# Performance work log

Hardware: AMD Instinct MI355X
Metric: run time of the kernel (lower is better)

Reference implementation:

```python
import jax, jax.numpy as jnp
import numpy as np

B, S, D, H = 4, 2048, 1024, 16
HD = D // H
ROPE_THETA = 10000.0


def setup_inputs() -> dict:
    key = jax.random.key(0)
    ks = jax.random.split(key, 5)
    scale = 1.0 / np.sqrt(D)
    inp = {
        "x": jax.random.normal(ks[0], (B, S, D), dtype=jnp.float32),
        "Wq": jax.random.normal(ks[1], (D, D), dtype=jnp.float32) * scale,
        "bq": jnp.zeros((D,), jnp.float32),
        "Wk": jax.random.normal(ks[2], (D, D), dtype=jnp.float32) * scale,
        "bk": jnp.zeros((D,), jnp.float32),
        "Wv": jax.random.normal(ks[3], (D, D), dtype=jnp.float32) * scale,
        "bv": jnp.zeros((D,), jnp.float32),
        "Wo": jax.random.normal(ks[4], (D, D), dtype=jnp.float32) * scale,
        "bo": jnp.zeros((D,), jnp.float32),
        # causal mask: True means masked (j > i), matching masked_fill semantics
        "attn_mask": jnp.triu(jnp.ones((S, S), dtype=bool), k=1),
    }
    return inp


def _rope(x):
    # x: [B, H, S, HD]; half-split rotary embedding
    half = HD // 2
    inv_freq = 1.0 / (ROPE_THETA ** (jnp.arange(0, half, dtype=jnp.float32) / half))
    pos = jnp.arange(x.shape[2], dtype=jnp.float32)
    freqs = pos[:, None] * inv_freq[None, :]            # [S, half]
    cos = jnp.cos(freqs)[None, None]                    # [1,1,S,half]
    sin = jnp.sin(freqs)[None, None]
    x1, x2 = x[..., :half], x[..., half:]
    return jnp.concatenate([x1 * cos - x2 * sin, x2 * cos + x1 * sin], axis=-1)


def reference(x, Wq, bq, Wk, bk, Wv, bv, Wo, bo, attn_mask):
    def shape(t):  # [B,S,D] -> [B,H,S,HD]
        return t.reshape(B, S, H, HD).transpose(0, 2, 1, 3)

    q = shape(x @ Wq.T + bq)
    k = shape(x @ Wk.T + bk)
    v = shape(x @ Wv.T + bv)
    q = _rope(q)
    k = _rope(k)
    scores = jnp.einsum("bhqd,bhkd->bhqk", q, k) * (HD ** -0.5)
    scores = jnp.where(attn_mask[None, None], -jnp.inf, scores)
    w = jax.nn.softmax(scores, axis=-1)
    attn = jnp.einsum("bhqk,bhkd->bhqd", w, v)
    merged = attn.transpose(0, 2, 1, 3).reshape(B, S, D)
    return merged @ Wo.T + bo
```

## Files before the change

kernel.cpp:

```cpp
#include <hip/hip_runtime.h>
#include <math.h>

#define BATCH 4
#define SEQ   2048
#define DMODEL 1024
#define NHEAD 16
#define HDIM  64
#define MROWS (BATCH*SEQ)

typedef unsigned short u16;
typedef unsigned int   u32;

using bf16x8 = __attribute__((ext_vector_type(8))) short;
using f32x4  = __attribute__((ext_vector_type(4))) float;
using f32x16 = __attribute__((ext_vector_type(16))) float;

__device__ __forceinline__ u16 f2bf(float f) {
    u32 u = __float_as_uint(f);
    u += 0x7fffu + ((u >> 16) & 1u);
    return (u16)(u >> 16);
}
__device__ __forceinline__ u32 pack2bf(float a, float b) {
    u32 ua = __float_as_uint(a); ua += 0x7fffu + ((ua >> 16) & 1u);
    u32 ub = __float_as_uint(b); ub += 0x7fffu + ((ub >> 16) & 1u);
    return (ua >> 16) | (ub & 0xffff0000u);
}

#define GLOBAL_LOAD_LDS16(gp, lp)                                              \
    __builtin_amdgcn_global_load_lds(                                          \
        (const __attribute__((address_space(1))) void*)(gp),                   \
        (__attribute__((address_space(3))) void*)(lp), 16, 0, 0)

__global__ __launch_bounds__(256) void convert_inputs(
    const float* __restrict__ x,  const float* __restrict__ wq,
    const float* __restrict__ wk, const float* __restrict__ wv,
    const float* __restrict__ wo, u16* __restrict__ dst)
{
    long long i4 = ((long long)blockIdx.x * 256 + threadIdx.x) * 4;
    const float* src; long long off;
    if (i4 < 8388608LL) { src = x; off = i4; }
    else {
        long long j = i4 - 8388608LL;
        int seg = (int)(j >> 20);
        off = j & 1048575LL;
        src = (seg == 0) ? wq : (seg == 1) ? wk : (seg == 2) ? wv : wo;
    }
    float4 v = *(const float4*)(src + off);
    u32 lo = (u32)f2bf(v.x) | ((u32)f2bf(v.y) << 16);
    u32 hi = (u32)f2bf(v.z) | ((u32)f2bf(v.w) << 16);
    *(uint2*)(dst + i4) = make_uint2(lo, hi);
}

template<int QKV>
__global__ __launch_bounds__(512) void gemm_mfma(
    const u16* __restrict__ A,
    const u16* __restrict__ Wq_, const u16* __restrict__ Wk_, const u16* __restrict__ Wv_,
    const float* __restrict__ bq_, const float* __restrict__ bk_, const float* __restrict__ bv_,
    u16* __restrict__ Cq_, u16* __restrict__ Ck_, u16* __restrict__ Cv_,
    float* __restrict__ Cf)
{
    __shared__ u16 As[3 * 256 * 64];
    __shared__ u16 Ws[3 * 128 * 64];

    const int t    = threadIdx.x;
    const int lane = t & 63;
    const int w    = t >> 6;
    const int quad = lane >> 4;
    const int l15  = lane & 15;
    const int wm   = w >> 1;
    const int wn   = w & 1;

    const int bx  = blockIdx.x;
    const int xcd = bx & 7;
    const int i_  = bx >> 3;
    const int bml = i_ & 3;
    const int n_  = i_ >> 2;
    const int seg = (QKV ? (n_ >> 3) : 0);
    const int nn  = (QKV ? (n_ & 7) : n_);

    const u16*   W    = (seg == 0) ? Wq_ : (seg == 1) ? Wk_ : Wv_;
    const float* bias = (seg == 0) ? bq_ : (seg == 1) ? bk_ : bv_;
    u16*         Cb   = (seg == 0) ? Cq_ : (seg == 1) ? Ck_ : Cv_;

    const int bm   = (xcd * 4 + bml) * 256;
    const int bn   = nn * 128;
    const int wrow = wm * 64;
    const int wcol = wn * 64;

    const int sr8 = lane >> 3;
    const int scl = (lane & 7) ^ sr8;
    const u16* gA = A + (size_t)(bm + 8 * w + sr8) * DMODEL + scl * 8;
    const u16* gB = W + (size_t)(bn + 8 * w + sr8) * DMODEL + scl * 8;

#define STAGE_A(li, kt, bs)                                                    \
    GLOBAL_LOAD_LDS16(gA + (size_t)(li) * 64 * DMODEL + (kt) * 64,             \
                      &As[(bs) * 16384 + ((li) * 64 + 8 * w) * 64])
#define STAGE_B(li, kt, bs)                                                    \
    GLOBAL_LOAD_LDS16(gB + (size_t)(li) * 64 * DMODEL + (kt) * 64,             \
                      &Ws[(bs) * 8192 + ((li) * 64 + 8 * w) * 64])

    STAGE_A(0, 0, 0); STAGE_A(1, 0, 0); STAGE_A(2, 0, 0); STAGE_A(3, 0, 0);
    STAGE_B(0, 0, 0); STAGE_B(1, 0, 0);
    STAGE_A(0, 1, 1); STAGE_A(1, 1, 1); STAGE_A(2, 1, 1); STAGE_A(3, 1, 1);
    STAGE_B(0, 1, 1); STAGE_B(1, 1, 1);
    asm volatile("s_waitcnt vmcnt(6)" ::: "memory");
    __builtin_amdgcn_s_barrier();

    const int c0 = (quad ^ (l15 & 7)) * 8;
    const int c1 = c0 ^ 32;

    f32x4 acc[4][4] = {};

    int bsel = 0;
    for (int kt = 0; kt < DMODEL / 64; ++kt) {
        const u16* Ab = &As[bsel * 16384];
        const u16* Bb = &Ws[bsel * 8192];
        const int  ks = kt + 2;
        const int  sb = (bsel >= 1) ? bsel - 1 : 2;
        const bool st = (ks < DMODEL / 64);

        bf16x8 af[4], bf[4];

        #pragma unroll
        for (int i = 0; i < 4; ++i)
            af[i] = *(const bf16x8*)&Ab[(wrow + 16 * i + l15) * 64 + c0];
        #pragma unroll
        for (int j = 0; j < 4; ++j)
            bf[j] = *(const bf16x8*)&Bb[(wcol + 16 * j + l15) * 64 + c0];
        if (st) { STAGE_A(0, ks, sb); STAGE_A(1, ks, sb); STAGE_A(2, ks, sb); }
        __builtin_amdgcn_s_barrier();
        __builtin_amdgcn_s_setprio(1);
        #pragma unroll
        for (int i = 0; i < 4; ++i)
            #pragma unroll
            for (int j = 0; j < 4; ++j)
                acc[i][j] = __builtin_amdgcn_mfma_f32_16x16x32_bf16(af[i], bf[j], acc[i][j], 0, 0, 0);
        __builtin_amdgcn_s_setprio(0);
        __builtin_amdgcn_s_barrier();

        #pragma unroll
        for (int i = 0; i < 4; ++i)
            af[i] = *(const bf16x8*)&Ab[(wrow + 16 * i + l15) * 64 + c1];
        #pragma unroll
        for (int j = 0; j < 4; ++j)
            bf[j] = *(const bf16x8*)&Bb[(wcol + 16 * j + l15) * 64 + c1];
        if (st) { STAGE_A(3, ks, sb); STAGE_B(0, ks, sb); STAGE_B(1, ks, sb); }
        __builtin_amdgcn_s_barrier();
        __builtin_amdgcn_s_setprio(1);
        #pragma unroll
        for (int i = 0; i < 4; ++i)
            #pragma unroll
            for (int j = 0; j < 4; ++j)
                acc[i][j] = __builtin_amdgcn_mfma_f32_16x16x32_bf16(af[i], bf[j], acc[i][j], 0, 0, 0);
        __builtin_amdgcn_s_setprio(0);
        if (st) asm volatile("s_waitcnt vmcnt(6)" ::: "memory");
        else    asm volatile("s_waitcnt vmcnt(0)" ::: "memory");
        __builtin_amdgcn_s_barrier();

        bsel = (bsel == 2) ? 0 : bsel + 1;
    }
#undef STAGE_A
#undef STAGE_B

    float bv[4];
    #pragma unroll
    for (int j = 0; j < 4; j++) bv[j] = bias[bn + wcol + 16 * j + l15];

    if constexpr (QKV == 0) {
        #pragma unroll
        for (int i = 0; i < 4; i++)
            #pragma unroll
            for (int r = 0; r < 4; r++) {
                int mg = bm + wrow + 16 * i + quad * 4 + r;
                #pragma unroll
                for (int j = 0; j < 4; j++)
                    Cf[(size_t)mg * DMODEL + bn + wcol + 16 * j + l15] = acc[i][j][r] + bv[j];
            }
    } else {
        if (seg == 2) {
            #pragma unroll
            for (int i = 0; i < 4; i++)
                #pragma unroll
                for (int r = 0; r < 4; r++) {
                    int mg = bm + wrow + 16 * i + quad * 4 + r;
                    #pragma unroll
                    for (int j = 0; j < 4; j++)
                        Cb[(size_t)mg * DMODEL + bn + wcol + 16 * j + l15] = f2bf(acc[i][j][r] + bv[j]);
                }
        } else {
            const float qscale = (seg == 0) ? 0.125f : 1.0f;
            float inv[2];
            #pragma unroll
            for (int j = 0; j < 2; j++) {
                int d = 16 * j + l15;
                inv[j] = exp2f(-(float)d * 0.4152410118609203f);
            }
            #pragma unroll
            for (int i = 0; i < 4; i++)
                #pragma unroll
                for (int r = 0; r < 4; r++) {
                    int mg = bm + wrow + 16 * i + quad * 4 + r;
                    int s  = mg & (SEQ - 1);
                    #pragma unroll
                    for (int j = 0; j < 2; j++) {
                        float f = (float)s * inv[j];
                        float sn, cs;
                        __sincosf(f, &sn, &cs);
                        float a1 = acc[i][j][r]     + bv[j];
                        float a2 = acc[i][j + 2][r] + bv[j + 2];
                        float o1 = (a1 * cs - a2 * sn) * qscale;
                        float o2 = (a2 * cs + a1 * sn) * qscale;
                        Cb[(size_t)mg * DMODEL + bn + wcol + 16 * j       + l15] = f2bf(o1);
                        Cb[(size_t)mg * DMODEL + bn + wcol + 16 * (j + 2) + l15] = f2bf(o2);
                    }
                }
        }
    }
}

__global__ __launch_bounds__(256) void attn_mfma(
    const u16* __restrict__ Q, const u16* __restrict__ K,
    const u16* __restrict__ V, u16* __restrict__ O)
{
    __shared__ u16 Qs[128 * 64];
    __shared__ u16 Ks[64 * 64];
    __shared__ u16 Vt[64 * 64];
    __shared__ u16 Ps[128 * 64];
    __shared__ float lS[128];

    const int t    = threadIdx.x;
    const int lane = t & 63;
    const int w    = t >> 6;
    const int l31  = lane & 31;
    const int hl   = lane >> 5;
    const int bid  = blockIdx.x;
    const int bh   = bid & 63;
    const int qt   = 15 - (bid >> 6);
    const int h    = bh & (NHEAD - 1);
    const int b    = bh >> 4;
    const int q0   = qt * 128;

    const size_t gbase = ((size_t)b * SEQ) * DMODEL + h * HDIM;

    {
        int rl = lane >> 3, cp = lane & 7;
        int c  = cp ^ rl;
        #pragma unroll
        for (int i = 0; i < 4; i++) {
            int row = 32 * w + 8 * i + rl;
            GLOBAL_LOAD_LDS16(Q + gbase + (size_t)(q0 + row) * DMODEL + c * 8,
                              &Qs[(32 * w + 8 * i) * 64]);
        }
    }
    __syncthreads();

    bf16x8 qf[4];
    {
        int row = 32 * w + l31;
        #pragma unroll
        for (int s = 0; s < 4; s++) {
            int c = (hl + 2 * s) ^ (row & 7);
            qf[s] = *(const bf16x8*)&Qs[row * 64 + c * 8];
        }
    }

    float lsum = 0.0f;
    f32x16 oacc[2] = {};

    const int ktn = 2 * qt + 2;
    for (int kt = 0; kt < ktn; kt++) {
        const int k0 = kt * 64;
        __syncthreads();

        {
            int rl = lane >> 3, cp = lane & 7;
            int c  = cp ^ rl;
            #pragma unroll
            for (int i = 0; i < 2; i++) {
                int row = 16 * w + 8 * i + rl;
                GLOBAL_LOAD_LDS16(K + gbase + (size_t)(k0 + row) * DMODEL + c * 8,
                                  &Ks[(16 * w + 8 * i) * 64]);
            }
        }
        {
            int j0 = (t & 31) * 2, d0 = (t >> 5) * 8;
            uint4 va = *(const uint4*)(V + gbase + (size_t)(k0 + j0)     * DMODEL + d0);
            uint4 vb = *(const uint4*)(V + gbase + (size_t)(k0 + j0 + 1) * DMODEL + d0);
            const u16* pa = (const u16*)&va;
            const u16* pb = (const u16*)&vb;
            int jd = t & 31, pos = jd & 3, ch = jd >> 2;
            #pragma unroll
            for (int e = 0; e < 8; e++) {
                int row = d0 + e;
                int pcch = ch ^ (row & 7);
                *(u32*)&Vt[row * 64 + pcch * 8 + pos * 2] = (u32)pa[e] | ((u32)pb[e] << 16);
            }
        }
        __syncthreads();

        const bool act = (k0 <= q0 + 32 * w + 31);
        if (act) {
            const int qrow = 32 * w + l31;
            const int qg   = q0 + qrow;
            #pragma unroll
            for (int krh = 0; krh < 2; krh++) {
                const bool qact = (k0 + 32 * krh <= q0 + 32 * w + 31);
                if (!qact) {
                    #pragma unroll
                    for (int g = 0; g < 4; g++)
                        #pragma unroll
                        for (int pp = 0; pp < 2; pp++) {
                            int kr = 32 * krh + 8 * g + 4 * hl + 2 * pp;
                            int jd = kr >> 1;
                            int pcc = (jd >> 2) ^ (qrow & 7);
                            *(u32*)&Ps[qrow * 64 + pcc * 8 + (jd & 3) * 2] = 0u;
                        }
                    continue;
                }
                f32x16 s = {};
                #pragma unroll
                for (int stp = 0; stp < 4; stp++) {
                    int row = 32 * krh + l31;
                    int c   = (hl + 2 * stp) ^ (l31 & 7);
                    bf16x8 ka = *(const bf16x8*)&Ks[row * 64 + c * 8];
                    s = __builtin_amdgcn_mfma_f32_32x32x16_bf16(ka, qf[stp], s, 0, 0, 0);
                }
                if (k0 + 32 * krh + 31 > q0 + 32 * w) {
                    #pragma unroll
                    for (int r = 0; r < 16; r++) {
                        int krg = k0 + 32 * krh + (r & 3) + 8 * (r >> 2) + 4 * hl;
                        if (krg > qg) s[r] = -1e30f;
                    }
                }
                float pv[16];
                #pragma unroll
                for (int r = 0; r < 16; r++) { pv[r] = __expf(s[r]); lsum += pv[r]; }
                #pragma unroll
                for (int g = 0; g < 4; g++)
                    #pragma unroll
                    for (int pp = 0; pp < 2; pp++) {
                        int kr = 32 * krh + 8 * g + 4 * hl + 2 * pp;
                        int jd = kr >> 1;
                        int pcc = (jd >> 2) ^ (qrow & 7);
                        *(u32*)&Ps[qrow * 64 + pcc * 8 + (jd & 3) * 2] =
                            pack2bf(pv[4 * g + 2 * pp], pv[4 * g + 2 * pp + 1]);
                    }
            }

            #pragma unroll
            for (int stp = 0; stp < 4; stp++) {
                int c = (hl + 2 * stp) ^ (l31 & 7);
                bf16x8 pf = *(const bf16x8*)&Ps[qrow * 64 + c * 8];
                #pragma unroll
                for (int dh = 0; dh < 2; dh++) {
                    bf16x8 vf = *(const bf16x8*)&Vt[(32 * dh + l31) * 64 + c * 8];
                    oacc[dh] = __builtin_amdgcn_mfma_f32_32x32x16_bf16(pf, vf, oacc[dh], 0, 0, 0);
                }
            }
        }
    }

    lsum += __shfl_xor(lsum, 32, 64);
    if (lane < 32) lS[32 * w + lane] = lsum;
    __syncthreads();

    #pragma unroll
    for (int g = 0; g < 4; g++) {
        f32x4 lv = *(const f32x4*)&lS[32 * w + 8 * g + 4 * hl];
        #pragma unroll
        for (int rr = 0; rr < 4; rr++) {
            int qg = q0 + 32 * w + rr + 8 * g + 4 * hl;
            float inv = 1.0f / lv[rr];
            #pragma unroll
            for (int dh = 0; dh < 2; dh++) {
                float o = oacc[dh][4 * g + rr] * inv;
                O[gbase + (size_t)qg * DMODEL + 32 * dh + l31] = f2bf(o);
            }
        }
    }
}

extern "C" void kernel_launch(void* const* d_in, const int* in_sizes, int n_in,
                              void* d_out, int out_size, void* d_ws, size_t ws_size,
                              hipStream_t stream)
{
    const float* x  = (const float*)d_in[0];
    const float* Wq = (const float*)d_in[1];
    const float* bq = (const float*)d_in[2];
    const float* Wk = (const float*)d_in[3];
    const float* bk = (const float*)d_in[4];
    const float* Wv = (const float*)d_in[5];
    const float* bv = (const float*)d_in[6];
    const float* Wo = (const float*)d_in[7];
    const float* bo = (const float*)d_in[8];

    u16* wsp = (u16*)d_ws;
    u16* xb  = wsp;
    u16* Wqb = wsp + 8388608;
    u16* Wkb = Wqb + 1048576;
    u16* Wvb = Wkb + 1048576;
    u16* Wob = Wvb + 1048576;
    u16* Qb  = Wob + 1048576;
    u16* Kb  = Qb + 8388608;
    u16* Vb  = Kb + 8388608;
    u16* Ab  = Vb + 8388608;

    convert_inputs<<<12288, 256, 0, stream>>>(x, Wq, Wk, Wv, Wo, xb);

    gemm_mfma<1><<<768, 512, 0, stream>>>(xb, Wqb, Wkb, Wvb, bq, bk, bv,
                                          Qb, Kb, Vb, nullptr);

    attn_mfma<<<1024, 256, 0, stream>>>(Qb, Kb, Vb, Ab);

    gemm_mfma<0><<<256, 512, 0, stream>>>(Ab, Wob, nullptr, nullptr, bo, nullptr, nullptr,
                                          nullptr, nullptr, nullptr, (float*)d_out);
}
```

Measured before the change: 263.4 us.

## Double-buffer K/V in attention, pre-transpose V in projection, keep P in registers

The V projection epilogue now stages results through LDS and writes V transposed as [B,H,HD,S], so the attention kernel can load V tiles directly into LDS with async global_load_lds. K and V tiles are double-buffered, with the next tile prefetched while the current one is computed, and there is a single barrier per iteration. The P matrix is packed with v_cvt_pk_bf16 and rearranged with permlane32_swap in registers instead of going through LDS. Also in the change: exp is replaced by exp2 with log2e folded into the Q scale, priority hints are set around the MFMAs, and the block order is reshuffled for better load balance. The new code relies on the aliasing of Qs with the second buffer being safe after the added sync, and on the ISA-specific asm instructions.

New measurement: 254.6 us. -3.3%, faster.

```diff
diff --git a/kernel.cpp b/kernel.cpp
--- a/kernel.cpp
+++ b/kernel.cpp
@@ -14,6 +14,7 @@
 using bf16x8 = __attribute__((ext_vector_type(8))) short;
 using f32x4  = __attribute__((ext_vector_type(4))) float;
 using f32x16 = __attribute__((ext_vector_type(16))) float;
+using u32x4  = __attribute__((ext_vector_type(4))) unsigned int;
 
 __device__ __forceinline__ u16 f2bf(float f) {
     u32 u = __float_as_uint(f);
@@ -25,6 +26,12 @@
     u32 ub = __float_as_uint(b); ub += 0x7fffu + ((ub >> 16) & 1u);
     return (ua >> 16) | (ub & 0xffff0000u);
 }
+__device__ __forceinline__ u32 cvtpk(float a, float b) {
+    u32 r;
+    asm("v_cvt_pk_bf16_f32 %0, %1, %2" : "=v"(r) : "v"(a), "v"(b));
+    return r;
+}
+#define PLSWAP(a, b) asm("v_permlane32_swap_b32 %0, %1" : "+v"(a), "+v"(b))
 
 #define GLOBAL_LOAD_LDS16(gp, lp)                                              \
     __builtin_amdgcn_global_load_lds(                                          \
@@ -178,17 +185,36 @@
             }
     } else {
         if (seg == 2) {
-            #pragma unroll
-            for (int i = 0; i < 4; i++)
+            u16* T = As;
+            #pragma unroll
+            for (int i = 0; i < 4; i++) {
                 #pragma unroll
-                for (int r = 0; r < 4; r++) {
-                    int mg = bm + wrow + 16 * i + quad * 4 + r;
-                    #pragma unroll
-                    for (int j = 0; j < 4; j++)
-                        Cb[(size_t)mg * DMODEL + bn + wcol + 16 * j + l15] = f2bf(acc[i][j][r] + bv[j]);
+                for (int j = 0; j < 4; j++) {
+                    int col = wrow + 16 * i + quad * 4;
+                    int row = wcol + 16 * j + l15;
+                    u32 lo = pack2bf(acc[i][j][0] + bv[j], acc[i][j][1] + bv[j]);
+                    u32 hi = pack2bf(acc[i][j][2] + bv[j], acc[i][j][3] + bv[j]);
+                    *(uint2*)((char*)T + row * 512 + ((col * 2) ^ ((row & 3) << 4)))
+                        = make_uint2(lo, hi);
                 }
+            }
+            __syncthreads();
+            {
+                int row  = t >> 2, colc = t & 3;
+                int hgl  = (bn + row) >> 6;
+                int dl   = (bn + row) & 63;
+                int bb   = bm >> 11;
+                size_t obase = (((size_t)(bb * NHEAD + hgl)) * HDIM + dl) * SEQ
+                             + (bm & (SEQ - 1)) + colc * 64;
+                #pragma unroll
+                for (int k = 0; k < 8; k++) {
+                    uint4 vv = *(const uint4*)((const char*)T + row * 512
+                                 + ((colc * 128 + k * 16) ^ ((row & 3) << 4)));
+                    *(uint4*)(Cb + obase + k * 8) = vv;
+                }
+            }
         } else {
-            const float qscale = (seg == 0) ? 0.125f : 1.0f;
+            const float qscale = (seg == 0) ? 0.18033688011112042f : 1.0f;
             float inv[2];
             #pragma unroll
             for (int j = 0; j < 2; j++) {
@@ -220,13 +246,15 @@
 
 __global__ __launch_bounds__(256) void attn_mfma(
     const u16* __restrict__ Q, const u16* __restrict__ K,
-    const u16* __restrict__ V, u16* __restrict__ O)
+    const u16* __restrict__ VT, u16* __restrict__ O)
 {
-    __shared__ u16 Qs[128 * 64];
-    __shared__ u16 Ks[64 * 64];
-    __shared__ u16 Vt[64 * 64];
-    __shared__ u16 Ps[128 * 64];
-    __shared__ float lS[128];
+    __shared__ __align__(16) u16 smem[16640];
+    u16* const Qs  = smem;
+    u16* const Ks0 = smem + 8192;
+    u16* const Ks1 = smem;
+    u16* const Vt0 = smem + 12288;
+    u16* const Vt1 = smem + 4096;
+    float* const lS = (float*)(smem + 16384);
 
     const int t    = threadIdx.x;
     const int lane = t & 63;
@@ -235,22 +263,32 @@
     const int hl   = lane >> 5;
     const int bid  = blockIdx.x;
     const int bh   = bid & 63;
-    const int qt   = 15 - (bid >> 6);
+    const int x_   = bid >> 6, g_ = x_ >> 2, r_ = x_ & 3;
+    const int qt   = (g_ == 0) ? 15 - r_ : (g_ == 1) ? 8 + r_
+                   : (g_ == 2) ? 4 + r_ : 3 - r_;
     const int h    = bh & (NHEAD - 1);
     const int b    = bh >> 4;
     const int q0   = qt * 128;
 
     const size_t gbase = ((size_t)b * SEQ) * DMODEL + h * HDIM;
-
-    {
-        int rl = lane >> 3, cp = lane & 7;
-        int c  = cp ^ rl;
-        #pragma unroll
-        for (int i = 0; i < 4; i++) {
-            int row = 32 * w + 8 * i + rl;
-            GLOBAL_LOAD_LDS16(Q + gbase + (size_t)(q0 + row) * DMODEL + c * 8,
-                              &Qs[(32 * w + 8 * i) * 64]);
-        }
+    const size_t vbase = ((size_t)(b * NHEAD + h)) * HDIM * SEQ;
+
+    const int rl  = lane >> 3;
+    const int csw = (lane & 7) ^ rl;
+
+    #pragma unroll
+    for (int i = 0; i < 4; i++) {
+        int row = 32 * w + 8 * i + rl;
+        GLOBAL_LOAD_LDS16(Q + gbase + (size_t)(q0 + row) * DMODEL + csw * 8,
+                          &Qs[(32 * w + 8 * i) * 64]);
+    }
+    #pragma unroll
+    for (int i = 0; i < 2; i++) {
+        int row = 16 * w + 8 * i + rl;
+        GLOBAL_LOAD_LDS16(K + gbase + (size_t)row * DMODEL + csw * 8,
+                          &Ks0[(16 * w + 8 * i) * 64]);
+        GLOBAL_LOAD_LDS16(VT + vbase + (size_t)row * SEQ + csw * 8,
+                          &Vt0[(16 * w + 8 * i) * 64]);
     }
     __syncthreads();
 
@@ -263,102 +301,94 @@
             qf[s] = *(const bf16x8*)&Qs[row * 64 + c * 8];
         }
     }
+    __syncthreads();
 
     float lsum = 0.0f;
     f32x16 oacc[2] = {};
+    const int qg   = q0 + 32 * w + l31;
+    const int qmax = q0 + 32 * w + 31;
+
+#define QUADRANT(KRH, F0, F1) do {                                             \
+    f32x16 s_ = {};                                                            \
+    __builtin_amdgcn_s_setprio(1);                                             \
+    _Pragma("unroll")                                                          \
+    for (int stp_ = 0; stp_ < 4; ++stp_) {                                     \
+        int c_ = ((hl + 2 * stp_) ^ (l31 & 7)) * 8;                            \
+        bf16x8 ka_ = *(const bf16x8*)&Ksb[(32 * (KRH) + l31) * 64 + c_];       \
+        s_ = __builtin_amdgcn_mfma_f32_32x32x16_bf16(ka_, qf[stp_], s_, 0, 0, 0);\
+    }                                                                          \
+    __builtin_amdgcn_s_setprio(0);                                             \
+    if (k0 + 32 * (KRH) + 31 > q0 + 32 * w) {                                  \
+        _Pragma("unroll")                                                      \
+        for (int rr_ = 0; rr_ < 16; ++rr_) {                                   \
+            int krg_ = k0 + 32 * (KRH) + (rr_ & 3) + 8 * (rr_ >> 2) + 4 * hl;  \
+            if (krg_ > qg) s_[rr_] = -1e30f;                                   \
+        }                                                                      \
+    }                                                                          \
+    float pv_[16];                                                             \
+    _Pragma("unroll")                                                          \
+    for (int rr_ = 0; rr_ < 16; ++rr_) pv_[rr_] = __builtin_amdgcn_exp2f(s_[rr_]);\
+    lsum += ((pv_[0]+pv_[1])+(pv_[2]+pv_[3])) + ((pv_[4]+pv_[5])+(pv_[6]+pv_[7]))\
+          + ((pv_[8]+pv_[9])+(pv_[10]+pv_[11])) + ((pv_[12]+pv_[13])+(pv_[14]+pv_[15]));\
+    u32 k01_ = cvtpk(pv_[0], pv_[1]),   k23_ = cvtpk(pv_[2], pv_[3]);          \
+    u32 k45_ = cvtpk(pv_[4], pv_[5]),   k67_ = cvtpk(pv_[6], pv_[7]);          \
+    u32 k89_ = cvtpk(pv_[8], pv_[9]),   kab_ = cvtpk(pv_[10], pv_[11]);        \
+    u32 kcd_ = cvtpk(pv_[12], pv_[13]), kef_ = cvtpk(pv_[14], pv_[15]);        \
+    PLSWAP(k01_, k45_); PLSWAP(k23_, k67_);                                    \
+    PLSWAP(k89_, kcd_); PLSWAP(kab_, kef_);                                    \
+    { union { u32x4 u; bf16x8 v; } c0_; c0_.u = (u32x4){k01_, k23_, k45_, k67_};\
+      F0 = c0_.v; }                                                            \
+    { union { u32x4 u; bf16x8 v; } c1_; c1_.u = (u32x4){k89_, kab_, kcd_, kef_};\
+      F1 = c1_.v; }                                                            \
+} while (0)
+
+#define PVSTEP(STP, PF) do {                                                   \
+    int c_ = ((hl + 2 * (STP)) ^ (l31 & 7)) * 8;                               \
+    bf16x8 v0_ = *(const bf16x8*)&Vtb[l31 * 64 + c_];                          \
+    bf16x8 v1_ = *(const bf16x8*)&Vtb[(32 + l31) * 64 + c_];                   \
+    oacc[0] = __builtin_amdgcn_mfma_f32_32x32x16_bf16(PF, v0_, oacc[0], 0, 0, 0);\
+    oacc[1] = __builtin_amdgcn_mfma_f32_32x32x16_bf16(PF, v1_, oacc[1], 0, 0, 0);\
+} while (0)
 
     const int ktn = 2 * qt + 2;
     for (int kt = 0; kt < ktn; kt++) {
         const int k0 = kt * 64;
-        __syncthreads();
-
-        {
-            int rl = lane >> 3, cp = lane & 7;
-            int c  = cp ^ rl;
+        u16* const Ksb = (kt & 1) ? Ks1 : Ks0;
+        u16* const Vtb = (kt & 1) ? Vt1 : Vt0;
+
+        if (kt + 1 < ktn) {
+            u16* const Ksn = (kt & 1) ? Ks0 : Ks1;
+            u16* const Vtn = (kt & 1) ? Vt0 : Vt1;
+            const size_t kk0 = (size_t)(kt + 1) * 64;
             #pragma unroll
             for (int i = 0; i < 2; i++) {
                 int row = 16 * w + 8 * i + rl;
-                GLOBAL_LOAD_LDS16(K + gbase + (size_t)(k0 + row) * DMODEL + c * 8,
-                                  &Ks[(16 * w + 8 * i) * 64]);
+                GLOBAL_LOAD_LDS16(K + gbase + (kk0 + row) * DMODEL + csw * 8,
+                                  &Ksn[(16 * w + 8 * i) * 64]);
+                GLOBAL_LOAD_LDS16(VT + vbase + (size_t)row * SEQ + kk0 + csw * 8,
+                                  &Vtn[(16 * w + 8 * i) * 64]);
             }
         }
-        {
-            int j0 = (t & 31) * 2, d0 = (t >> 5) * 8;
-            uint4 va = *(const uint4*)(V + gbase + (size_t)(k0 + j0)     * DMODEL + d0);
-            uint4 vb = *(const uint4*)(V + gbase + (size_t)(k0 + j0 + 1) * DMODEL + d0);
-            const u16* pa = (const u16*)&va;
-            const u16* pb = (const u16*)&vb;
-            int jd = t & 31, pos = jd & 3, ch = jd >> 2;
-            #pragma unroll
-            for (int e = 0; e < 8; e++) {
-                int row = d0 + e;
-                int pcch = ch ^ (row & 7);
-                *(u32*)&Vt[row * 64 + pcch * 8 + pos * 2] = (u32)pa[e] | ((u32)pb[e] << 16);
+
+        if (k0 <= qmax) {
+            const bool q2 = (k0 + 32 <= qmax);
+            bf16x8 pa0, pa1, pa2, pa3;
+            QUADRANT(0, pa0, pa1);
+            __builtin_amdgcn_s_setprio(1);
+            PVSTEP(0, pa0); PVSTEP(1, pa1);
+            __builtin_amdgcn_s_setprio(0);
+            if (q2) {
+                QUADRANT(1, pa2, pa3);
+                __builtin_amdgcn_s_setprio(1);
+                PVSTEP(2, pa2); PVSTEP(3, pa3);
+                __builtin_amdgcn_s_setprio(0);
             }
         }
-        __syncthreads();
-
-        const bool act = (k0 <= q0 + 32 * w + 31);
-        if (act) {
-            const int qrow = 32 * w + l31;
-            const int qg   = q0 + qrow;
-            #pragma unroll
-            for (int krh = 0; krh < 2; krh++) {
-                const bool qact = (k0 + 32 * krh <= q0 + 32 * w + 31);
-                if (!qact) {
-                    #pragma unroll
-                    for (int g = 0; g < 4; g++)
-                        #pragma unroll
-                        for (int pp = 0; pp < 2; pp++) {
-                            int kr = 32 * krh + 8 * g + 4 * hl + 2 * pp;
-                            int jd = kr >> 1;
-                            int pcc = (jd >> 2) ^ (qrow & 7);
-                            *(u32*)&Ps[qrow * 64 + pcc * 8 + (jd & 3) * 2] = 0u;
-                        }
-                    continue;
-                }
-                f32x16 s = {};
-                #pragma unroll
-                for (int stp = 0; stp < 4; stp++) {
-                    int row = 32 * krh + l31;
-                    int c   = (hl + 2 * stp) ^ (l31 & 7);
-                    bf16x8 ka = *(const bf16x8*)&Ks[row * 64 + c * 8];
-                    s = __builtin_amdgcn_mfma_f32_32x32x16_bf16(ka, qf[stp], s, 0, 0, 0);
-                }
-                if (k0 + 32 * krh + 31 > q0 + 32 * w) {
-                    #pragma unroll
-                    for (int r = 0; r < 16; r++) {
-                        int krg = k0 + 32 * krh + (r & 3) + 8 * (r >> 2) + 4 * hl;
-                        if (krg > qg) s[r] = -1e30f;
-                    }
-                }
-                float pv[16];
-                #pragma unroll
-                for (int r = 0; r < 16; r++) { pv[r] = __expf(s[r]); lsum += pv[r]; }
-                #pragma unroll
-                for (int g = 0; g < 4; g++)
-                    #pragma unroll
-                    for (int pp = 0; pp < 2; pp++) {
-                        int kr = 32 * krh + 8 * g + 4 * hl + 2 * pp;
-                        int jd = kr >> 1;
-                        int pcc = (jd >> 2) ^ (qrow & 7);
-                        *(u32*)&Ps[qrow * 64 + pcc * 8 + (jd & 3) * 2] =
-                            pack2bf(pv[4 * g + 2 * pp], pv[4 * g + 2 * pp + 1]);
-                    }
-            }
-
-            #pragma unroll
-            for (int stp = 0; stp < 4; stp++) {
-                int c = (hl + 2 * stp) ^ (l31 & 7);
-                bf16x8 pf = *(const bf16x8*)&Ps[qrow * 64 + c * 8];
-                #pragma unroll
-                for (int dh = 0; dh < 2; dh++) {
-                    bf16x8 vf = *(const bf16x8*)&Vt[(32 * dh + l31) * 64 + c * 8];
-                    oacc[dh] = __builtin_amdgcn_mfma_f32_32x32x16_bf16(pf, vf, oacc[dh], 0, 0, 0);
-                }
-            }
-        }
-    }
+        asm volatile("s_waitcnt vmcnt(0)" ::: "memory");
+        __builtin_amdgcn_s_barrier();
+    }
+#undef QUADRANT
+#undef PVSTEP
 
     lsum += __shfl_xor(lsum, 32, 64);
     if (lane < 32) lS[32 * w + lane] = lsum;
@@ -369,12 +399,12 @@
         f32x4 lv = *(const f32x4*)&lS[32 * w + 8 * g + 4 * hl];
         #pragma unroll
         for (int rr = 0; rr < 4; rr++) {
-            int qg = q0 + 32 * w + rr + 8 * g + 4 * hl;
+            int qg2 = q0 + 32 * w + rr + 8 * g + 4 * hl;
             float inv = 1.0f / lv[rr];
             #pragma unroll
             for (int dh = 0; dh < 2; dh++) {
                 float o = oacc[dh][4 * g + rr] * inv;
-                O[gbase + (size_t)qg * DMODEL + 32 * dh + l31] = f2bf(o);
+                O[gbase + (size_t)qg2 * DMODEL + 32 * dh + l31] = f2bf(o);
             }
         }
     }
```
